# Optimization experiments

Hardware: AMD Instinct MI355X
Metric: run time of the kernel (lower is better)

The kernel has to match this reference:

```python
import jax, jax.numpy as jnp
from jax import lax
import numpy as np

T, B, INPUT_SIZE, HIDDEN, LAYERS, OUT_DIM = 256, 1000, 300, 2, 2, 1


def setup_inputs() -> dict:
    key = jax.random.key(0)
    ks = jax.random.split(key, 12)
    H4 = 4 * HIDDEN
    s = 0.1
    return {
        "x": jax.random.normal(ks[0], (T, B, INPUT_SIZE), dtype=jnp.float32),
        "h0": jnp.zeros((LAYERS, B, HIDDEN), dtype=jnp.float32),
        "c0": jnp.zeros((LAYERS, B, HIDDEN), dtype=jnp.float32),
        "W_ih0": jax.random.normal(ks[1], (H4, INPUT_SIZE), dtype=jnp.float32) * s,
        "W_hh0": jax.random.normal(ks[2], (H4, HIDDEN), dtype=jnp.float32) * s,
        "b_ih0": jax.random.normal(ks[3], (H4,), dtype=jnp.float32) * s,
        "b_hh0": jax.random.normal(ks[4], (H4,), dtype=jnp.float32) * s,
        "W_ih1": jax.random.normal(ks[5], (H4, HIDDEN), dtype=jnp.float32) * s,
        "W_hh1": jax.random.normal(ks[6], (H4, HIDDEN), dtype=jnp.float32) * s,
        "b_ih1": jax.random.normal(ks[7], (H4,), dtype=jnp.float32) * s,
        "b_hh1": jax.random.normal(ks[8], (H4,), dtype=jnp.float32) * s,
        "W_lin": jax.random.normal(ks[9], (OUT_DIM, HIDDEN), dtype=jnp.float32) * s,
        "b_lin": jax.random.normal(ks[10], (OUT_DIM,), dtype=jnp.float32) * s,
    }


def _lstm_layer(x, h0, c0, W_ih, W_hh, b_ih, b_hh):
    # x: [T, B, D_in]; PyTorch gate order i, f, g, o.
    # Precompute input projections for all timesteps at once (one big GEMM).
    xg = jnp.einsum('tbd,gd->tbg', x, W_ih) + (b_ih + b_hh)  # [T, B, 4H]

    def step(carry, xt):
        h, c = carry
        gates = xt + h @ W_hh.T  # [B, 4H]
        i, f, g, o = jnp.split(gates, 4, axis=-1)
        c = jax.nn.sigmoid(f) * c + jax.nn.sigmoid(i) * jnp.tanh(g)
        h = jax.nn.sigmoid(o) * jnp.tanh(c)
        return (h, c), h

    (_, _), ys = lax.scan(step, (h0, c0), xg)
    return ys  # [T, B, H]


def reference(x, h0, c0, W_ih0, W_hh0, b_ih0, b_hh0, W_ih1, W_hh1, b_ih1, b_hh1, W_lin, b_lin):
    y0 = _lstm_layer(x, h0[0], c0[0], W_ih0, W_hh0, b_ih0, b_hh0)   # [T, B, H]
    y1 = _lstm_layer(y0, h0[1], c0[1], W_ih1, W_hh1, b_ih1, b_hh1)  # [T, B, H]
    pred = y1[-1] @ W_lin.T + b_lin  # [B, 1]
    return pred.reshape(-1)          # [B]
```

## Files before the change

### kernel.cpp

```cpp
#include <hip/hip_runtime.h>

#define T_STEPS 256
#define BATCH   1000
#define D_IN    300
#define H4      8
#define ROWS_PER_BLK 32

__global__ __launch_bounds__(256) void xproj_kernel(
    const float* __restrict__ x, const float* __restrict__ W,
    const float* __restrict__ b_ih, const float* __restrict__ b_hh,
    float* __restrict__ xg)
{
    __shared__ __align__(16) float xs[ROWS_PER_BLK * D_IN];
    __shared__ __align__(16) float ws[H4 * D_IN];

    const int tid = threadIdx.x;

    const float4* __restrict__ xin = (const float4*)(x + (long)blockIdx.x * (ROWS_PER_BLK * D_IN));
    float4* xs4 = (float4*)xs;
    for (int k = tid; k < ROWS_PER_BLK * D_IN / 4; k += 256)
        xs4[k] = xin[k];

    const float4* __restrict__ win = (const float4*)W;
    float4* ws4 = (float4*)ws;
    for (int k = tid; k < H4 * D_IN / 4; k += 256)
        ws4[k] = win[k];

    __syncthreads();

    const int r = tid >> 3;
    const int g = tid & 7;
    const float4* __restrict__ xr = (const float4*)(xs + r * D_IN);
    const float4* __restrict__ wr = (const float4*)(ws + g * D_IN);

    float a0 = 0.f, a1 = 0.f, a2 = 0.f, a3 = 0.f;
#pragma unroll 5
    for (int k = 0; k < D_IN / 4; ++k) {
        float4 xv = xr[k];
        float4 wv = wr[k];
        a0 += xv.x * wv.x;
        a1 += xv.y * wv.y;
        a2 += xv.z * wv.z;
        a3 += xv.w * wv.w;
    }
    xg[(long)blockIdx.x * 256 + tid] = (a0 + a1) + (a2 + a3) + b_ih[g] + b_hh[g];
}

__device__ __forceinline__ float sigf(float x) {
    return __builtin_amdgcn_rcpf(1.0f + __expf(-x));
}
__device__ __forceinline__ float tanhfast(float x) {
    return fmaf(-2.0f, __builtin_amdgcn_rcpf(1.0f + __expf(2.0f * x)), 1.0f);
}

__global__ __launch_bounds__(64) void lstm_seq_kernel(
    const float* __restrict__ xg,
    const float* __restrict__ h0in, const float* __restrict__ c0in,
    const float* __restrict__ Whh0, const float* __restrict__ Wih1,
    const float* __restrict__ Whh1, const float* __restrict__ bih1,
    const float* __restrict__ bhh1, const float* __restrict__ Wlin,
    const float* __restrict__ blin, float* __restrict__ out)
{
    int b = blockIdx.x * 64 + threadIdx.x;
    bool active = (b < BATCH);
    int bb = active ? b : (BATCH - 1);

    float whh0[H4][2], wih1[H4][2], whh1[H4][2], bias1[H4];
#pragma unroll
    for (int k = 0; k < H4; ++k) {
        whh0[k][0] = Whh0[2 * k]; whh0[k][1] = Whh0[2 * k + 1];
        wih1[k][0] = Wih1[2 * k]; wih1[k][1] = Wih1[2 * k + 1];
        whh1[k][0] = Whh1[2 * k]; whh1[k][1] = Whh1[2 * k + 1];
        bias1[k]   = bih1[k] + bhh1[k];
    }

    float h0a = h0in[2 * bb],             h0b = h0in[2 * bb + 1];
    float c0a = c0in[2 * bb],             c0b = c0in[2 * bb + 1];
    float h1a = h0in[2 * BATCH + 2 * bb], h1b = h0in[2 * BATCH + 2 * bb + 1];
    float c1a = c0in[2 * BATCH + 2 * bb], c1b = c0in[2 * BATCH + 2 * bb + 1];

    const float4* __restrict__ xp = (const float4*)xg;

    float4 plo[4], phi[4];
#pragma unroll
    for (int t = 0; t < 4; ++t) {
        plo[t] = xp[(t * BATCH + bb) * 2];
        phi[t] = xp[(t * BATCH + bb) * 2 + 1];
    }

    float p[H4];
#pragma unroll
    for (int k = 0; k < H4; ++k)
        p[k] = bias1[k] + h1a * whh1[k][0] + h1b * whh1[k][1];

#pragma unroll 4
    for (int t = 0; t < T_STEPS; ++t) {
        int s = t & 3;
        float4 l4 = plo[s], h4 = phi[s];
        if (t + 4 < T_STEPS) {
            plo[s] = xp[((t + 4) * BATCH + bb) * 2];
            phi[s] = xp[((t + 4) * BATCH + bb) * 2 + 1];
        }
        float xv[H4] = {l4.x, l4.y, l4.z, l4.w, h4.x, h4.y, h4.z, h4.w};

        float gt[H4];
#pragma unroll
        for (int k = 0; k < H4; ++k)
            gt[k] = xv[k] + h0a * whh0[k][0] + h0b * whh0[k][1];
        c0a = sigf(gt[2]) * c0a + sigf(gt[0]) * tanhfast(gt[4]);
        c0b = sigf(gt[3]) * c0b + sigf(gt[1]) * tanhfast(gt[5]);
        h0a = sigf(gt[6]) * tanhfast(c0a);
        h0b = sigf(gt[7]) * tanhfast(c0b);

        float qt[H4];
#pragma unroll
        for (int k = 0; k < H4; ++k)
            qt[k] = p[k] + h0a * wih1[k][0] + h0b * wih1[k][1];
        c1a = sigf(qt[2]) * c1a + sigf(qt[0]) * tanhfast(qt[4]);
        c1b = sigf(qt[3]) * c1b + sigf(qt[1]) * tanhfast(qt[5]);
        h1a = sigf(qt[6]) * tanhfast(c1a);
        h1b = sigf(qt[7]) * tanhfast(c1b);

#pragma unroll
        for (int k = 0; k < H4; ++k)
            p[k] = bias1[k] + h1a * whh1[k][0] + h1b * whh1[k][1];
    }

    if (active)
        out[b] = h1a * Wlin[0] + h1b * Wlin[1] + blin[0];
}

extern "C" void kernel_launch(void* const* d_in, const int* in_sizes, int n_in,
                              void* d_out, int out_size, void* d_ws, size_t ws_size,
                              hipStream_t stream) {
    const float* x      = (const float*)d_in[0];
    const float* h0     = (const float*)d_in[1];
    const float* c0     = (const float*)d_in[2];
    const float* W_ih0  = (const float*)d_in[3];
    const float* W_hh0  = (const float*)d_in[4];
    const float* b_ih0  = (const float*)d_in[5];
    const float* b_hh0  = (const float*)d_in[6];
    const float* W_ih1  = (const float*)d_in[7];
    const float* W_hh1  = (const float*)d_in[8];
    const float* b_ih1  = (const float*)d_in[9];
    const float* b_hh1  = (const float*)d_in[10];
    const float* W_lin  = (const float*)d_in[11];
    const float* b_lin  = (const float*)d_in[12];
    float* out = (float*)d_out;
    float* xg  = (float*)d_ws;

    const int rows = T_STEPS * BATCH;
    xproj_kernel<<<rows / ROWS_PER_BLK, 256, 0, stream>>>(x, W_ih0, b_ih0, b_hh0, xg);
    lstm_seq_kernel<<<(BATCH + 63) / 64, 64, 0, stream>>>(
        xg, h0, c0, W_hh0, W_ih1, W_hh1, b_ih1, b_hh1, W_lin, b_lin, out);
}
```

Measured before the change: 577.0 us.

## Double-buffer xproj tiles via async LDS loads and fold log2e into weights

The input-projection kernel becomes a persistent kernel of 1000 blocks, each processing 8 row tiles. It uses global_load_lds direct-to-LDS copies, double-buffered so the next tile loads while the current one is computed. Separately, the log2(e) factors (doubled for the tanh gates) are pre-multiplied into the projected inputs, recurrent weights and biases, so the activations can call exp2 directly. That removes a multiply from each transcendental on the serial recurrence chain. The risks are the hand-written vmcnt/barrier synchronisation and a small change in numerical rounding.

```diff
diff --git a/kernel.cpp b/kernel.cpp
--- a/kernel.cpp
+++ b/kernel.cpp
@@ -4,53 +4,103 @@
 #define BATCH   1000
 #define D_IN    300
 #define H4      8
-#define ROWS_PER_BLK 32
+#define ROWS    32
+#define TILE_F4 2400
+#define NT      8
+#define NBLK    1000
+
+#define L2E   1.4426950408889634f
+#define L2E2  2.8853900817779268f
+
+__device__ __forceinline__ float fexp2(float x) {
+#if __has_builtin(__builtin_amdgcn_exp2f)
+    return __builtin_amdgcn_exp2f(x);
+#else
+    return exp2f(x);
+#endif
+}
+__device__ __forceinline__ float sig2(float x) {
+    return __builtin_amdgcn_rcpf(1.0f + fexp2(-x));
+}
+__device__ __forceinline__ float tanh2(float x) {
+    return fmaf(-2.0f, __builtin_amdgcn_rcpf(1.0f + fexp2(x)), 1.0f);
+}
+
+__device__ __forceinline__ void gload16(const float4* g, float4* l) {
+    __builtin_amdgcn_global_load_lds(
+        (const __attribute__((address_space(1))) void*)g,
+        (__attribute__((address_space(3))) void*)l, 16, 0, 0);
+}
 
 __global__ __launch_bounds__(256) void xproj_kernel(
     const float* __restrict__ x, const float* __restrict__ W,
     const float* __restrict__ b_ih, const float* __restrict__ b_hh,
     float* __restrict__ xg)
 {
-    __shared__ __align__(16) float xs[ROWS_PER_BLK * D_IN];
-    __shared__ __align__(16) float ws[H4 * D_IN];
-
-    const int tid = threadIdx.x;
-
-    const float4* __restrict__ xin = (const float4*)(x + (long)blockIdx.x * (ROWS_PER_BLK * D_IN));
-    float4* xs4 = (float4*)xs;
-    for (int k = tid; k < ROWS_PER_BLK * D_IN / 4; k += 256)
-        xs4[k] = xin[k];
-
-    const float4* __restrict__ win = (const float4*)W;
-    float4* ws4 = (float4*)ws;
-    for (int k = tid; k < H4 * D_IN / 4; k += 256)
-        ws4[k] = win[k];
-
-    __syncthreads();
-
+    __shared__ __align__(16) float xs[2][2560 * 4];
+    __shared__ __align__(16) float ws[768 * 4];
+
+    const int tid   = threadIdx.x;
+    const int wbase = tid & ~63;
+
+    const float4* xf4 = (const float4*)x;
+    const float4* wf4 = (const float4*)W;
+    float4* xs0 = (float4*)xs[0];
+    float4* xs1 = (float4*)xs[1];
+    float4* wsf = (float4*)ws;
+
+    const long tile0 = (long)blockIdx.x * NT;
+
+    const int g = tid & 7;
     const int r = tid >> 3;
-    const int g = tid & 7;
-    const float4* __restrict__ xr = (const float4*)(xs + r * D_IN);
-    const float4* __restrict__ wr = (const float4*)(ws + g * D_IN);
-
-    float a0 = 0.f, a1 = 0.f, a2 = 0.f, a3 = 0.f;
+    const float bias  = b_ih[g] + b_hh[g];
+    const float scale = (g == 4 || g == 5) ? L2E2 : L2E;
+
+#pragma unroll
+    for (int j = 0; j < 3; ++j) {
+        int k  = j * 256 + tid;
+        int gk = k < 600 ? k : 599;
+        gload16(wf4 + gk, wsf + (j * 256 + wbase));
+    }
+#pragma unroll
+    for (int j = 0; j < 10; ++j) {
+        int k  = j * 256 + tid;
+        int gk = k < TILE_F4 ? k : TILE_F4 - 1;
+        gload16(xf4 + tile0 * TILE_F4 + gk, xs0 + (j * 256 + wbase));
+    }
+    asm volatile("s_waitcnt vmcnt(0)" ::: "memory");
+    __builtin_amdgcn_s_barrier();
+
+    const float4* wr = wsf + g * 75;
+
+    for (int i = 0; i < NT; ++i) {
+        if (i + 1 < NT) {
+            float4* nbuf = (i & 1) ? xs0 : xs1;
+            long tb = (tile0 + i + 1) * TILE_F4;
+#pragma unroll
+            for (int j = 0; j < 10; ++j) {
+                int k  = j * 256 + tid;
+                int gk = k < TILE_F4 ? k : TILE_F4 - 1;
+                gload16(xf4 + tb + gk, nbuf + (j * 256 + wbase));
+            }
+        }
+
+        const float4* xr = ((i & 1) ? xs1 : xs0) + r * 75;
+        float a0 = 0.f, a1 = 0.f, a2 = 0.f, a3 = 0.f;
 #pragma unroll 5
-    for (int k = 0; k < D_IN / 4; ++k) {
-        float4 xv = xr[k];
-        float4 wv = wr[k];
-        a0 += xv.x * wv.x;
-        a1 += xv.y * wv.y;
-        a2 += xv.z * wv.z;
-        a3 += xv.w * wv.w;
-    }
-    xg[(long)blockIdx.x * 256 + tid] = (a0 + a1) + (a2 + a3) + b_ih[g] + b_hh[g];
-}
-
-__device__ __forceinline__ float sigf(float x) {
-    return __builtin_amdgcn_rcpf(1.0f + __expf(-x));
-}
-__device__ __forceinline__ float tanhfast(float x) {
-    return fmaf(-2.0f, __builtin_amdgcn_rcpf(1.0f + __expf(2.0f * x)), 1.0f);
+        for (int k = 0; k < 75; ++k) {
+            float4 xv = xr[k];
+            float4 wv = wr[k];
+            a0 += xv.x * wv.x; a1 += xv.y * wv.y;
+            a2 += xv.z * wv.z; a3 += xv.w * wv.w;
+        }
+        xg[(tile0 + i) * 256 + tid] = ((a0 + a1) + (a2 + a3) + bias) * scale;
+
+        if (i + 1 < NT) {
+            asm volatile("s_waitcnt vmcnt(1)" ::: "memory");
+            __builtin_amdgcn_s_barrier();
+        }
+    }
 }
 
 __global__ __launch_bounds__(64) void lstm_seq_kernel(
@@ -68,10 +118,11 @@
     float whh0[H4][2], wih1[H4][2], whh1[H4][2], bias1[H4];
 #pragma unroll
     for (int k = 0; k < H4; ++k) {
-        whh0[k][0] = Whh0[2 * k]; whh0[k][1] = Whh0[2 * k + 1];
-        wih1[k][0] = Wih1[2 * k]; wih1[k][1] = Wih1[2 * k + 1];
-        whh1[k][0] = Whh1[2 * k]; whh1[k][1] = Whh1[2 * k + 1];
-        bias1[k]   = bih1[k] + bhh1[k];
+        float f = (k == 4 || k == 5) ? L2E2 : L2E;
+        whh0[k][0] = Whh0[2 * k] * f; whh0[k][1] = Whh0[2 * k + 1] * f;
+        wih1[k][0] = Wih1[2 * k] * f; wih1[k][1] = Wih1[2 * k + 1] * f;
+        whh1[k][0] = Whh1[2 * k] * f; whh1[k][1] = Whh1[2 * k + 1] * f;
+        bias1[k]   = (bih1[k] + bhh1[k]) * f;
     }
 
     float h0a = h0in[2 * bb],             h0b = h0in[2 * bb + 1];
@@ -107,19 +158,19 @@
 #pragma unroll
         for (int k = 0; k < H4; ++k)
             gt[k] = xv[k] + h0a * whh0[k][0] + h0b * whh0[k][1];
-        c0a = sigf(gt[2]) * c0a + sigf(gt[0]) * tanhfast(gt[4]);
-        c0b = sigf(gt[3]) * c0b + sigf(gt[1]) * tanhfast(gt[5]);
-        h0a = sigf(gt[6]) * tanhfast(c0a);
-        h0b = sigf(gt[7]) * tanhfast(c0b);
+        c0a = sig2(gt[2]) * c0a + sig2(gt[0]) * tanh2(gt[4]);
+        c0b = sig2(gt[3]) * c0b + sig2(gt[1]) * tanh2(gt[5]);
+        h0a = sig2(gt[6]) * tanh2(c0a * L2E2);
+        h0b = sig2(gt[7]) * tanh2(c0b * L2E2);
 
         float qt[H4];
 #pragma unroll
         for (int k = 0; k < H4; ++k)
             qt[k] = p[k] + h0a * wih1[k][0] + h0b * wih1[k][1];
-        c1a = sigf(qt[2]) * c1a + sigf(qt[0]) * tanhfast(qt[4]);
-        c1b = sigf(qt[3]) * c1b + sigf(qt[1]) * tanhfast(qt[5]);
-        h1a = sigf(qt[6]) * tanhfast(c1a);
-        h1b = sigf(qt[7]) * tanhfast(c1b);
+        c1a = sig2(qt[2]) * c1a + sig2(qt[0]) * tanh2(qt[4]);
+        c1b = sig2(qt[3]) * c1b + sig2(qt[1]) * tanh2(qt[5]);
+        h1a = sig2(qt[6]) * tanh2(c1a * L2E2);
+        h1b = sig2(qt[7]) * tanh2(c1b * L2E2);
 
 #pragma unroll
         for (int k = 0; k < H4; ++k)
@@ -149,8 +200,7 @@
     float* out = (float*)d_out;
     float* xg  = (float*)d_ws;
 
-    const int rows = T_STEPS * BATCH;
-    xproj_kernel<<<rows / ROWS_PER_BLK, 256, 0, stream>>>(x, W_ih0, b_ih0, b_hh0, xg);
+    xproj_kernel<<<NBLK, 256, 0, stream>>>(x, W_ih0, b_ih0, b_hh0, xg);
     lstm_seq_kernel<<<(BATCH + 63) / 64, 64, 0, stream>>>(
         xg, h0, c0, W_hh0, W_ih1, W_hh1, b_ih1, b_hh1, W_lin, b_lin, out);
 }
```

After: 588.5 us. 1.02x slower.
